# Performance work log

Measured on AMD Instinct MI355X. Metric: run time of the kernel, lower is better.

## Reference

```python
import jax, jax.numpy as jnp
import numpy as np

N_NODES = 100000
N_EDGES = 1600000
D = 128
BN_EPS = 1e-5

def setup_inputs() -> dict:
    key = jax.random.key(0)
    ks = jax.random.split(key, 6)
    h = jax.random.normal(ks[0], (N_NODES, D), dtype=jnp.float32)
    src = jax.random.randint(ks[1], (N_EDGES,), 0, N_NODES, dtype=jnp.int32)
    dst = jax.random.randint(ks[2], (N_EDGES,), 0, N_NODES, dtype=jnp.int32)
    eps = jnp.zeros((1,), dtype=jnp.float32)
    # 2-layer GIN apply_func MLP, scaled for stable activations
    W1 = jax.random.normal(ks[3], (D, D), dtype=jnp.float32) / np.sqrt(D)
    b1 = jnp.zeros((D,), dtype=jnp.float32)
    W2 = jax.random.normal(ks[4], (D, D), dtype=jnp.float32) / np.sqrt(D)
    b2 = jnp.zeros((D,), dtype=jnp.float32)
    gamma = jnp.ones((D,), dtype=jnp.float32)
    beta = jnp.zeros((D,), dtype=jnp.float32)
    return {"h": h, "src": src, "dst": dst, "eps": eps,
            "W1": W1, "b1": b1, "W2": W2, "b2": b2,
            "gamma": gamma, "beta": beta}

def reference(h, src, dst, eps, W1, b1, W2, b2, gamma, beta):
    # --- neighbor sum aggregation: update_all(copy_u('h'), fn.sum) ---
    msgs = h[src]                                   # [E, D] irregular gather
    neigh = jax.ops.segment_sum(msgs, dst, num_segments=N_NODES)  # [N, D]
    # --- eps-scaled self term ---
    x = (1.0 + eps[0]) * h + neigh                  # [N, D]
    # --- apply_func: 2-layer MLP ---
    x = jax.nn.relu(x @ W1 + b1)
    x = x @ W2 + b2
    # --- BatchNorm1d over node dim (training-mode batch stats) ---
    mean = jnp.mean(x, axis=0)
    var = jnp.mean(jnp.square(x - mean), axis=0)
    x = (x - mean) * jax.lax.rsqrt(var + BN_EPS) * gamma + beta
    # --- activation + residual ---
    x = jax.nn.relu(x)
    x = h + x  # residual (in_dim == out_dim)
    return x
```

## Files before the change

kernel.cpp:

```cpp
#include <hip/hip_runtime.h>

#define NN 100000
#define NE 1600000
#define DD 128
#define BN_EPS 1e-5f

#define NWIN 782
#define EPB 8192
#define NBLK ((NE + EPB - 1) / EPB)
#define CAP 3072

typedef __attribute__((ext_vector_type(8))) short short8;
typedef __attribute__((ext_vector_type(4))) float floatx4;

__device__ __forceinline__ unsigned short f2bf(float f) {
    union { float f; unsigned u; } v; v.f = f;
    return (unsigned short)((v.u + 0x7FFFu + ((v.u >> 16) & 1u)) >> 16);
}
__device__ __forceinline__ float bf2f(unsigned short u) {
    union { unsigned u; float f; } v; v.u = ((unsigned)u) << 16;
    return v.f;
}

__global__ __launch_bounds__(256) void prep_kernel(
    float* __restrict__ stats, int* __restrict__ wcnt,
    const float* __restrict__ W1, const float* __restrict__ W2,
    unsigned short* __restrict__ W1t, unsigned short* __restrict__ W2t,
    const float* __restrict__ h, unsigned short* __restrict__ hb, int do_hb)
{
    int tid0 = blockIdx.x * blockDim.x + threadIdx.x;
    int stride = gridDim.x * blockDim.x;
    if (tid0 < 2 * DD) stats[tid0] = 0.0f;
    if (tid0 < NWIN) wcnt[tid0] = 0;
    for (int i = tid0; i < DD * DD; i += stride) {
        int n = i >> 7, k = i & 127;
        W1t[i] = f2bf(W1[k * DD + n]);
        W2t[i] = f2bf(W2[k * DD + n]);
    }
    if (do_hb) {
        const float4* h4 = (const float4*)h;
        ushort4* hb4 = (ushort4*)hb;
        for (int i = tid0; i < NN * (DD / 4); i += stride) {
            float4 v = h4[i];
            ushort4 o;
            o.x = f2bf(v.x); o.y = f2bf(v.y); o.z = f2bf(v.z); o.w = f2bf(v.w);
            hb4[i] = o;
        }
    }
}

__global__ __launch_bounds__(256) void wscatter_kernel(
    const int* __restrict__ src, const int* __restrict__ dst,
    int* __restrict__ wcnt, int* __restrict__ estage)
{
    __shared__ int bins[NWIN];
    int blk = blockIdx.x, t = threadIdx.x;
    for (int j = t; j < NWIN; j += 256) bins[j] = 0;
    __syncthreads();
    int base = blk * EPB;
    int cnt = min(EPB, NE - base);
    for (int i = t; i < cnt; i += 256)
        atomicAdd(&bins[dst[base + i] >> 7], 1);
    __syncthreads();
    for (int j = t; j < NWIN; j += 256) {
        int c = bins[j];
        int b = (c > 0) ? atomicAdd(&wcnt[j], c) : 0;
        bins[j] = j * CAP + b;
    }
    __syncthreads();
    for (int i = t; i < cnt; i += 256) {
        int e = base + i;
        int d = dst[e];
        int pos = atomicAdd(&bins[d >> 7], 1);
        estage[pos] = (src[e] << 7) | (d & 127);
    }
}

__global__ __launch_bounds__(256) void wpermute_kernel(
    const int* __restrict__ wcnt, int* __restrict__ estage,
    int2* __restrict__ off2)
{
    __shared__ int ew[CAP];
    __shared__ int cnt[128];
    __shared__ int part[128];
    __shared__ int cur[128];
    int b = blockIdx.x, t = threadIdx.x;
    int wbase = b * CAP;
    int n = min(wcnt[b], CAP);
    if (t < 128) cnt[t] = 0;
    __syncthreads();
    for (int i = t; i < n; i += 256) {
        int e = estage[wbase + i];
        ew[i] = e;
        atomicAdd(&cnt[e & 127], 1);
    }
    __syncthreads();
    if (t < 128) part[t] = cnt[t];
    __syncthreads();
#pragma unroll
    for (int ofs = 1; ofs < 128; ofs <<= 1) {
        int u = (t < 128 && t >= ofs) ? part[t - ofs] : 0;
        __syncthreads();
        if (t < 128) part[t] += u;
        __syncthreads();
    }
    if (t < 128) {
        int excl = part[t] - cnt[t];
        cur[t] = wbase + excl;
        int node = (b << 7) + t;
        if (node < NN) off2[node] = make_int2(wbase + excl, wbase + excl + cnt[t]);
    }
    __syncthreads();
    for (int i = t; i < n; i += 256) {
        int e = ew[i];
        int pos = atomicAdd(&cur[e & 127], 1);
        estage[pos] = e >> 7;
    }
}

__global__ __launch_bounds__(256) void gather_bf16_kernel(
    const float* __restrict__ h, const unsigned short* __restrict__ hb,
    const float* __restrict__ eps, const int2* __restrict__ off2,
    const int* __restrict__ src_sorted, unsigned short* __restrict__ xb)
{
    int node = blockIdx.x * 16 + (threadIdx.x >> 4);
    if (node >= NN) return;
    int c8 = threadIdx.x & 15;
    const float s = 1.0f + eps[0];
    const float4* h4 = (const float4*)h;
    float4 a0 = h4[node * 32 + c8 * 2];
    float4 a1 = h4[node * 32 + c8 * 2 + 1];
    float acc[8] = {s * a0.x, s * a0.y, s * a0.z, s * a0.w,
                    s * a1.x, s * a1.y, s * a1.z, s * a1.w};
    int2 oo = off2[node];
    int e = oo.x, eend = oo.y;
    const short8* hb8 = (const short8*)hb;
    for (; e + 3 < eend; e += 4) {
        int s0 = src_sorted[e],     s1 = src_sorted[e + 1];
        int s2 = src_sorted[e + 2], s3 = src_sorted[e + 3];
        short8 v0 = hb8[s0 * 16 + c8];
        short8 v1 = hb8[s1 * 16 + c8];
        short8 v2 = hb8[s2 * 16 + c8];
        short8 v3 = hb8[s3 * 16 + c8];
#pragma unroll
        for (int j = 0; j < 8; ++j) {
            float t0 = bf2f((unsigned short)v0[j]) + bf2f((unsigned short)v1[j]);
            float t1 = bf2f((unsigned short)v2[j]) + bf2f((unsigned short)v3[j]);
            acc[j] += t0 + t1;
        }
    }
    for (; e < eend; ++e) {
        short8 v0 = hb8[src_sorted[e] * 16 + c8];
#pragma unroll
        for (int j = 0; j < 8; ++j) acc[j] += bf2f((unsigned short)v0[j]);
    }
    short8 o;
#pragma unroll
    for (int j = 0; j < 8; ++j) o[j] = (short)f2bf(acc[j]);
    ((short8*)xb)[node * 16 + c8] = o;
}

__global__ __launch_bounds__(256) void gather_f32_kernel(
    const float* __restrict__ h, const float* __restrict__ eps,
    const int2* __restrict__ off2, const int* __restrict__ src_sorted,
    unsigned short* __restrict__ xb)
{
    int node = blockIdx.x * 16 + (threadIdx.x >> 4);
    if (node >= NN) return;
    int c8 = threadIdx.x & 15;
    const float4* h4 = (const float4*)h;
    const float s = 1.0f + eps[0];
    float4 a0 = h4[node * 32 + c8 * 2];
    float4 a1 = h4[node * 32 + c8 * 2 + 1];
    float acc[8] = {s * a0.x, s * a0.y, s * a0.z, s * a0.w,
                    s * a1.x, s * a1.y, s * a1.z, s * a1.w};
    int2 oo = off2[node];
    int e = oo.x, eend = oo.y;
    for (; e + 1 < eend; e += 2) {
        int s0 = src_sorted[e], s1 = src_sorted[e + 1];
        float4 u0 = h4[s0 * 32 + c8 * 2], u1 = h4[s0 * 32 + c8 * 2 + 1];
        float4 w0 = h4[s1 * 32 + c8 * 2], w1 = h4[s1 * 32 + c8 * 2 + 1];
        acc[0] += u0.x + w0.x; acc[1] += u0.y + w0.y;
        acc[2] += u0.z + w0.z; acc[3] += u0.w + w0.w;
        acc[4] += u1.x + w1.x; acc[5] += u1.y + w1.y;
        acc[6] += u1.z + w1.z; acc[7] += u1.w + w1.w;
    }
    if (e < eend) {
        int s0 = src_sorted[e];
        float4 u0 = h4[s0 * 32 + c8 * 2], u1 = h4[s0 * 32 + c8 * 2 + 1];
        acc[0] += u0.x; acc[1] += u0.y; acc[2] += u0.z; acc[3] += u0.w;
        acc[4] += u1.x; acc[5] += u1.y; acc[6] += u1.z; acc[7] += u1.w;
    }
    short8 o;
#pragma unroll
    for (int j = 0; j < 8; ++j) o[j] = (short)f2bf(acc[j]);
    ((short8*)xb)[node * 16 + c8] = o;
}

__global__ __launch_bounds__(256) void mlp_fused_kernel(
    const unsigned short* __restrict__ X,
    const unsigned short* __restrict__ W1t, const unsigned short* __restrict__ W2t,
    const float* __restrict__ b1, const float* __restrict__ b2,
    unsigned short* __restrict__ Y, float* __restrict__ stats)
{
    extern __shared__ char smem[];
    unsigned short* wl = (unsigned short*)smem;
    unsigned short* xl = (unsigned short*)(smem + 34816);

    const int tid = threadIdx.x;
    const int r0 = blockIdx.x * 64;
    const int lane = tid & 63;
    const int wv = tid >> 6;
    const int m = lane & 15;
    const int hi = lane >> 4;

    const short8* W18 = (const short8*)W1t;
#pragma unroll
    for (int l = 0; l < 8; ++l) {
        int idx = tid + l * 256;
        int n = idx >> 4, c = idx & 15;
        *(short8*)&wl[n * 136 + c * 8] = W18[idx];
    }
    const short8* X8 = (const short8*)X;
#pragma unroll
    for (int l = 0; l < 4; ++l) {
        int idx = tid + l * 256;
        int row = idx >> 4, c = idx & 15;
        int g = r0 + row;
        short8 v = {0, 0, 0, 0, 0, 0, 0, 0};
        if (g < NN) v = X8[g * 16 + c];
        *(short8*)&xl[row * 136 + c * 8] = v;
    }
    __syncthreads();

    floatx4 acc[8];
#pragma unroll
    for (int i = 0; i < 8; ++i) acc[i] = (floatx4){0.f, 0.f, 0.f, 0.f};
#pragma unroll
    for (int kc = 0; kc < 4; ++kc) {
        short8 a = *(const short8*)&xl[(wv * 16 + m) * 136 + kc * 32 + hi * 8];
#pragma unroll
        for (int nt = 0; nt < 8; ++nt) {
            short8 b = *(const short8*)&wl[(nt * 16 + m) * 136 + kc * 32 + hi * 8];
            acc[nt] = __builtin_amdgcn_mfma_f32_16x16x32_bf16(a, b, acc[nt], 0, 0, 0);
        }
    }
    __syncthreads();

#pragma unroll
    for (int nt = 0; nt < 8; ++nt) {
        float bv = b1[nt * 16 + m];
#pragma unroll
        for (int r = 0; r < 4; ++r) {
            float v = fmaxf(acc[nt][r] + bv, 0.f);
            xl[(wv * 16 + hi * 4 + r) * 136 + nt * 16 + m] = f2bf(v);
        }
    }
    const short8* W28 = (const short8*)W2t;
#pragma unroll
    for (int l = 0; l < 8; ++l) {
        int idx = tid + l * 256;
        int n = idx >> 4, c = idx & 15;
        *(short8*)&wl[n * 136 + c * 8] = W28[idx];
    }
    __syncthreads();

#pragma unroll
    for (int i = 0; i < 8; ++i) acc[i] = (floatx4){0.f, 0.f, 0.f, 0.f};
#pragma unroll
    for (int kc = 0; kc < 4; ++kc) {
        short8 a = *(const short8*)&xl[(wv * 16 + m) * 136 + kc * 32 + hi * 8];
#pragma unroll
        for (int nt = 0; nt < 8; ++nt) {
            short8 b = *(const short8*)&wl[(nt * 16 + m) * 136 + kc * 32 + hi * 8];
            acc[nt] = __builtin_amdgcn_mfma_f32_16x16x32_bf16(a, b, acc[nt], 0, 0, 0);
        }
    }
    __syncthreads();

#pragma unroll
    for (int nt = 0; nt < 8; ++nt) {
        float bv = b2[nt * 16 + m];
#pragma unroll
        for (int r = 0; r < 4; ++r) {
            float v = acc[nt][r] + bv;
            xl[(wv * 16 + hi * 4 + r) * 136 + nt * 16 + m] = f2bf(v);
        }
    }
    __syncthreads();

#pragma unroll
    for (int l = 0; l < 4; ++l) {
        int idx = tid + l * 256;
        int row = idx >> 4, c = idx & 15;
        int g = r0 + row;
        if (g < NN)
            ((short8*)Y)[g * 16 + c] = *(const short8*)&xl[row * 136 + c * 8];
    }

    int col = tid & 127, half = tid >> 7;
    int rlim = min(64, NN - r0);
    int rbeg = half * 32, rend = min(rbeg + 32, rlim);
    float s = 0.f, q = 0.f;
    for (int r = rbeg; r < rend; ++r) {
        float v = bf2f(xl[r * 136 + col]);
        s += v; q += v * v;
    }
    float* red = (float*)wl;
    red[tid] = s;
    red[256 + tid] = q;
    __syncthreads();
    if (half == 0) {
        atomicAdd(&stats[col],      red[col] + red[128 + col]);
        atomicAdd(&stats[DD + col], red[256 + col] + red[256 + 128 + col]);
    }
}

__global__ __launch_bounds__(256) void bn_final_kernel(
    const unsigned short* __restrict__ Y, const float* __restrict__ h,
    const float* __restrict__ gamma, const float* __restrict__ beta,
    const float* __restrict__ stats, float* __restrict__ out)
{
    const float invN = 1.0f / (float)NN;
    const ushort4* Y4 = (const ushort4*)Y;
    const float4* H4 = (const float4*)h;
    float4* O4 = (float4*)out;
    const int total = NN * (DD / 4);
    for (int i = blockIdx.x * blockDim.x + threadIdx.x; i < total;
         i += gridDim.x * blockDim.x) {
        int cg = i & 31;
        int c = cg << 2;
        ushort4 u = Y4[i];
        float4 hv = H4[i];
        float4 g = ((const float4*)gamma)[cg];
        float4 bt = ((const float4*)beta)[cg];

        float m0 = stats[c + 0] * invN, m1 = stats[c + 1] * invN;
        float m2 = stats[c + 2] * invN, m3 = stats[c + 3] * invN;
        float v0 = stats[DD + c + 0] * invN - m0 * m0;
        float v1 = stats[DD + c + 1] * invN - m1 * m1;
        float v2 = stats[DD + c + 2] * invN - m2 * m2;
        float v3 = stats[DD + c + 3] * invN - m3 * m3;

        float4 r;
        r.x = hv.x + fmaxf((bf2f(u.x) - m0) * rsqrtf(v0 + BN_EPS) * g.x + bt.x, 0.f);
        r.y = hv.y + fmaxf((bf2f(u.y) - m1) * rsqrtf(v1 + BN_EPS) * g.y + bt.y, 0.f);
        r.z = hv.z + fmaxf((bf2f(u.z) - m2) * rsqrtf(v2 + BN_EPS) * g.z + bt.z, 0.f);
        r.w = hv.w + fmaxf((bf2f(u.w) - m3) * rsqrtf(v3 + BN_EPS) * g.w + bt.w, 0.f);
        O4[i] = r;
    }
}

extern "C" void kernel_launch(void* const* d_in, const int* in_sizes, int n_in,
                              void* d_out, int out_size, void* d_ws, size_t ws_size,
                              hipStream_t stream)
{
    const float* h     = (const float*)d_in[0];
    const int*   src   = (const int*)d_in[1];
    const int*   dst   = (const int*)d_in[2];
    const float* eps   = (const float*)d_in[3];
    const float* W1    = (const float*)d_in[4];
    const float* b1    = (const float*)d_in[5];
    const float* W2    = (const float*)d_in[6];
    const float* b2    = (const float*)d_in[7];
    const float* gamma = (const float*)d_in[8];
    const float* beta  = (const float*)d_in[9];
    float* out = (float*)d_out;

    char* w = (char*)d_ws;
    size_t o = 0;
    int2* off2      = (int2*)(w + o); o += (size_t)NN * 8;
    float* stats    = (float*)(w + o); o += 256 * 4;
    unsigned short* W1t = (unsigned short*)(w + o); o += (size_t)DD * DD * 2;
    unsigned short* W2t = (unsigned short*)(w + o); o += (size_t)DD * DD * 2;
    int* wcnt       = (int*)(w + o); o += 1024 * 4;
    int* estage     = (int*)(w + o); o += (size_t)NWIN * CAP * 4;
    unsigned short* xb  = (unsigned short*)(w + o); o += (size_t)NN * DD * 2;
    unsigned short* hb  = (unsigned short*)(w + o); o += (size_t)NN * DD * 2;
    const int use_hb = (ws_size >= o) ? 1 : 0;

    prep_kernel<<<512, 256, 0, stream>>>(stats, wcnt, W1, W2, W1t, W2t, h, hb, use_hb);

    wscatter_kernel<<<NBLK, 256, 0, stream>>>(src, dst, wcnt, estage);

    wpermute_kernel<<<NWIN, 256, 0, stream>>>(wcnt, estage, off2);

    if (use_hb)
        gather_bf16_kernel<<<(NN + 15) / 16, 256, 0, stream>>>(h, hb, eps, off2, estage, xb);
    else
        gather_f32_kernel<<<(NN + 15) / 16, 256, 0, stream>>>(h, eps, off2, estage, xb);

    int gemm_blocks = (NN + 63) / 64;
    size_t gemm_lds = 34816 + 17408;
    mlp_fused_kernel<<<gemm_blocks, 256, gemm_lds, stream>>>(xb, W1t, W2t, b1, b2, xb, stats);

    bn_final_kernel<<<1024, 256, 0, stream>>>(xb, h, gamma, beta, stats, out);
}
```

Measured before the change: 322.1 us.

## Fuse prep with edge scatter, fuse window permute with gather, streamline BN epilogue

The weight/h conversion now runs as extra blocks inside the edge-binning launch, and dst indices are cached in LDS for the second pass. The per-window permutation is merged into the gather kernel, which keeps sorted sources in LDS instead of writing them and an offset array back to global memory. The BN kernel precomputes per-column scale and shift and uses 8-wide loads. This saves launches and global round trips, but the gather runs with far fewer, larger blocks (128 nodes each), which may hurt load balance and latency hiding.

```diff
diff --git a/kernel.cpp b/kernel.cpp
--- a/kernel.cpp
+++ b/kernel.cpp
@@ -9,6 +9,9 @@
 #define EPB 8192
 #define NBLK ((NE + EPB - 1) / EPB)
 #define CAP 3072
+#define PREPBLKS 316
+#define GRID_PS (NBLK + PREPBLKS)
+#define BN_BLOCKS 1024
 
 typedef __attribute__((ext_vector_type(8))) short short8;
 typedef __attribute__((ext_vector_type(4))) float floatx4;
@@ -22,179 +25,169 @@
     return v.f;
 }
 
-__global__ __launch_bounds__(256) void prep_kernel(
-    float* __restrict__ stats, int* __restrict__ wcnt,
+__global__ __launch_bounds__(256) void prep_scatter_kernel(
+    float* __restrict__ stats,
     const float* __restrict__ W1, const float* __restrict__ W2,
     unsigned short* __restrict__ W1t, unsigned short* __restrict__ W2t,
-    const float* __restrict__ h, unsigned short* __restrict__ hb, int do_hb)
-{
-    int tid0 = blockIdx.x * blockDim.x + threadIdx.x;
-    int stride = gridDim.x * blockDim.x;
-    if (tid0 < 2 * DD) stats[tid0] = 0.0f;
-    if (tid0 < NWIN) wcnt[tid0] = 0;
-    for (int i = tid0; i < DD * DD; i += stride) {
-        int n = i >> 7, k = i & 127;
-        W1t[i] = f2bf(W1[k * DD + n]);
-        W2t[i] = f2bf(W2[k * DD + n]);
-    }
-    if (do_hb) {
-        const float4* h4 = (const float4*)h;
-        ushort4* hb4 = (ushort4*)hb;
-        for (int i = tid0; i < NN * (DD / 4); i += stride) {
-            float4 v = h4[i];
-            ushort4 o;
-            o.x = f2bf(v.x); o.y = f2bf(v.y); o.z = f2bf(v.z); o.w = f2bf(v.w);
-            hb4[i] = o;
-        }
-    }
-}
-
-__global__ __launch_bounds__(256) void wscatter_kernel(
+    const float* __restrict__ h, unsigned short* __restrict__ hb, int do_hb,
     const int* __restrict__ src, const int* __restrict__ dst,
     int* __restrict__ wcnt, int* __restrict__ estage)
 {
     __shared__ int bins[NWIN];
-    int blk = blockIdx.x, t = threadIdx.x;
-    for (int j = t; j < NWIN; j += 256) bins[j] = 0;
-    __syncthreads();
-    int base = blk * EPB;
-    int cnt = min(EPB, NE - base);
-    for (int i = t; i < cnt; i += 256)
-        atomicAdd(&bins[dst[base + i] >> 7], 1);
-    __syncthreads();
-    for (int j = t; j < NWIN; j += 256) {
-        int c = bins[j];
-        int b = (c > 0) ? atomicAdd(&wcnt[j], c) : 0;
-        bins[j] = j * CAP + b;
-    }
-    __syncthreads();
-    for (int i = t; i < cnt; i += 256) {
-        int e = base + i;
-        int d = dst[e];
-        int pos = atomicAdd(&bins[d >> 7], 1);
-        estage[pos] = (src[e] << 7) | (d & 127);
-    }
-}
-
-__global__ __launch_bounds__(256) void wpermute_kernel(
-    const int* __restrict__ wcnt, int* __restrict__ estage,
-    int2* __restrict__ off2)
+    __shared__ int dstl[EPB];
+    int t = threadIdx.x;
+
+    if (blockIdx.x < NBLK) {
+        int blk = blockIdx.x;
+        for (int j = t; j < NWIN; j += 256) bins[j] = 0;
+        __syncthreads();
+        int base = blk * EPB;
+        int cnt = min(EPB, NE - base);
+        for (int i = t; i < cnt; i += 256) {
+            int d = dst[base + i];
+            dstl[i] = d;
+            atomicAdd(&bins[d >> 7], 1);
+        }
+        __syncthreads();
+        for (int j = t; j < NWIN; j += 256) {
+            int c = bins[j];
+            int b = (c > 0) ? atomicAdd(&wcnt[j], c) : 0;
+            bins[j] = j * CAP + b;
+        }
+        __syncthreads();
+        for (int i = t; i < cnt; i += 256) {
+            int d = dstl[i];
+            int pos = atomicAdd(&bins[d >> 7], 1);
+            estage[pos] = (src[base + i] << 7) | (d & 127);
+        }
+    } else {
+        int tid0 = (blockIdx.x - NBLK) * 256 + t;
+        int stride = PREPBLKS * 256;
+        if (tid0 < 2 * DD) stats[tid0] = 0.0f;
+        for (int i = tid0; i < DD * DD; i += stride) {
+            int n = i >> 7, k = i & 127;
+            W1t[i] = f2bf(W1[k * DD + n]);
+            W2t[i] = f2bf(W2[k * DD + n]);
+        }
+        if (do_hb) {
+            const float4* h4 = (const float4*)h;
+            ushort4* hb4 = (ushort4*)hb;
+            for (int i = tid0; i < NN * (DD / 4); i += stride) {
+                float4 v = h4[i];
+                ushort4 o;
+                o.x = f2bf(v.x); o.y = f2bf(v.y); o.z = f2bf(v.z); o.w = f2bf(v.w);
+                hb4[i] = o;
+            }
+        }
+    }
+}
+
+template <bool HB>
+__global__ __launch_bounds__(512) void permgather_kernel(
+    const float* __restrict__ h, const unsigned short* __restrict__ hb,
+    const float* __restrict__ eps, const int* __restrict__ wcnt,
+    const int* __restrict__ estage, unsigned short* __restrict__ xb)
 {
     __shared__ int ew[CAP];
+    __shared__ int es[CAP];
     __shared__ int cnt[128];
-    __shared__ int part[128];
+    __shared__ int scn[128];
+    __shared__ int begS[128];
+    __shared__ int endS[128];
     __shared__ int cur[128];
+
     int b = blockIdx.x, t = threadIdx.x;
+    if (t < 128) cnt[t] = 0;
+    __syncthreads();
+
+    int n = min(wcnt[b], CAP);
     int wbase = b * CAP;
-    int n = min(wcnt[b], CAP);
-    if (t < 128) cnt[t] = 0;
-    __syncthreads();
-    for (int i = t; i < n; i += 256) {
+    for (int i = t; i < n; i += 512) {
         int e = estage[wbase + i];
         ew[i] = e;
         atomicAdd(&cnt[e & 127], 1);
     }
     __syncthreads();
-    if (t < 128) part[t] = cnt[t];
+
+    if (t < 128) scn[t] = cnt[t];
     __syncthreads();
 #pragma unroll
     for (int ofs = 1; ofs < 128; ofs <<= 1) {
-        int u = (t < 128 && t >= ofs) ? part[t - ofs] : 0;
-        __syncthreads();
-        if (t < 128) part[t] += u;
+        int u = (t < 128 && t >= ofs) ? scn[t - ofs] : 0;
+        __syncthreads();
+        if (t < 128) scn[t] += u;
         __syncthreads();
     }
     if (t < 128) {
-        int excl = part[t] - cnt[t];
-        cur[t] = wbase + excl;
-        int node = (b << 7) + t;
-        if (node < NN) off2[node] = make_int2(wbase + excl, wbase + excl + cnt[t]);
-    }
-    __syncthreads();
-    for (int i = t; i < n; i += 256) {
+        int excl = scn[t] - cnt[t];
+        begS[t] = excl;
+        endS[t] = excl + cnt[t];
+        cur[t] = excl;
+    }
+    __syncthreads();
+
+    for (int i = t; i < n; i += 512) {
         int e = ew[i];
         int pos = atomicAdd(&cur[e & 127], 1);
-        estage[pos] = e >> 7;
-    }
-}
-
-__global__ __launch_bounds__(256) void gather_bf16_kernel(
-    const float* __restrict__ h, const unsigned short* __restrict__ hb,
-    const float* __restrict__ eps, const int2* __restrict__ off2,
-    const int* __restrict__ src_sorted, unsigned short* __restrict__ xb)
-{
-    int node = blockIdx.x * 16 + (threadIdx.x >> 4);
-    if (node >= NN) return;
-    int c8 = threadIdx.x & 15;
-    const float s = 1.0f + eps[0];
+        es[pos] = e >> 7;
+    }
+    __syncthreads();
+
+    const float sE = 1.0f + eps[0];
     const float4* h4 = (const float4*)h;
-    float4 a0 = h4[node * 32 + c8 * 2];
-    float4 a1 = h4[node * 32 + c8 * 2 + 1];
-    float acc[8] = {s * a0.x, s * a0.y, s * a0.z, s * a0.w,
-                    s * a1.x, s * a1.y, s * a1.z, s * a1.w};
-    int2 oo = off2[node];
-    int e = oo.x, eend = oo.y;
     const short8* hb8 = (const short8*)hb;
-    for (; e + 3 < eend; e += 4) {
-        int s0 = src_sorted[e],     s1 = src_sorted[e + 1];
-        int s2 = src_sorted[e + 2], s3 = src_sorted[e + 3];
-        short8 v0 = hb8[s0 * 16 + c8];
-        short8 v1 = hb8[s1 * 16 + c8];
-        short8 v2 = hb8[s2 * 16 + c8];
-        short8 v3 = hb8[s3 * 16 + c8];
-#pragma unroll
-        for (int j = 0; j < 8; ++j) {
-            float t0 = bf2f((unsigned short)v0[j]) + bf2f((unsigned short)v1[j]);
-            float t1 = bf2f((unsigned short)v2[j]) + bf2f((unsigned short)v3[j]);
-            acc[j] += t0 + t1;
-        }
-    }
-    for (; e < eend; ++e) {
-        short8 v0 = hb8[src_sorted[e] * 16 + c8];
-#pragma unroll
-        for (int j = 0; j < 8; ++j) acc[j] += bf2f((unsigned short)v0[j]);
-    }
-    short8 o;
-#pragma unroll
-    for (int j = 0; j < 8; ++j) o[j] = (short)f2bf(acc[j]);
-    ((short8*)xb)[node * 16 + c8] = o;
-}
-
-__global__ __launch_bounds__(256) void gather_f32_kernel(
-    const float* __restrict__ h, const float* __restrict__ eps,
-    const int2* __restrict__ off2, const int* __restrict__ src_sorted,
-    unsigned short* __restrict__ xb)
-{
-    int node = blockIdx.x * 16 + (threadIdx.x >> 4);
-    if (node >= NN) return;
-    int c8 = threadIdx.x & 15;
-    const float4* h4 = (const float4*)h;
-    const float s = 1.0f + eps[0];
-    float4 a0 = h4[node * 32 + c8 * 2];
-    float4 a1 = h4[node * 32 + c8 * 2 + 1];
-    float acc[8] = {s * a0.x, s * a0.y, s * a0.z, s * a0.w,
-                    s * a1.x, s * a1.y, s * a1.z, s * a1.w};
-    int2 oo = off2[node];
-    int e = oo.x, eend = oo.y;
-    for (; e + 1 < eend; e += 2) {
-        int s0 = src_sorted[e], s1 = src_sorted[e + 1];
-        float4 u0 = h4[s0 * 32 + c8 * 2], u1 = h4[s0 * 32 + c8 * 2 + 1];
-        float4 w0 = h4[s1 * 32 + c8 * 2], w1 = h4[s1 * 32 + c8 * 2 + 1];
-        acc[0] += u0.x + w0.x; acc[1] += u0.y + w0.y;
-        acc[2] += u0.z + w0.z; acc[3] += u0.w + w0.w;
-        acc[4] += u1.x + w1.x; acc[5] += u1.y + w1.y;
-        acc[6] += u1.z + w1.z; acc[7] += u1.w + w1.w;
-    }
-    if (e < eend) {
-        int s0 = src_sorted[e];
-        float4 u0 = h4[s0 * 32 + c8 * 2], u1 = h4[s0 * 32 + c8 * 2 + 1];
-        acc[0] += u0.x; acc[1] += u0.y; acc[2] += u0.z; acc[3] += u0.w;
-        acc[4] += u1.x; acc[5] += u1.y; acc[6] += u1.z; acc[7] += u1.w;
-    }
-    short8 o;
-#pragma unroll
-    for (int j = 0; j < 8; ++j) o[j] = (short)f2bf(acc[j]);
-    ((short8*)xb)[node * 16 + c8] = o;
+    int c8 = t & 15;
+#pragma unroll
+    for (int pass = 0; pass < 4; ++pass) {
+        int nl = pass * 32 + (t >> 4);
+        int node = (b << 7) + nl;
+        if (node >= NN) continue;
+        float4 a0 = h4[node * 32 + c8 * 2];
+        float4 a1 = h4[node * 32 + c8 * 2 + 1];
+        float acc[8] = {sE * a0.x, sE * a0.y, sE * a0.z, sE * a0.w,
+                        sE * a1.x, sE * a1.y, sE * a1.z, sE * a1.w};
+        int e = begS[nl], eend = endS[nl];
+        if (HB) {
+            for (; e + 3 < eend; e += 4) {
+                int s0 = es[e], s1 = es[e + 1], s2 = es[e + 2], s3 = es[e + 3];
+                short8 v0 = hb8[s0 * 16 + c8];
+                short8 v1 = hb8[s1 * 16 + c8];
+                short8 v2 = hb8[s2 * 16 + c8];
+                short8 v3 = hb8[s3 * 16 + c8];
+#pragma unroll
+                for (int j = 0; j < 8; ++j) {
+                    float t0 = bf2f((unsigned short)v0[j]) + bf2f((unsigned short)v1[j]);
+                    float t1 = bf2f((unsigned short)v2[j]) + bf2f((unsigned short)v3[j]);
+                    acc[j] += t0 + t1;
+                }
+            }
+            for (; e < eend; ++e) {
+                short8 v0 = hb8[es[e] * 16 + c8];
+#pragma unroll
+                for (int j = 0; j < 8; ++j) acc[j] += bf2f((unsigned short)v0[j]);
+            }
+        } else {
+            for (; e + 1 < eend; e += 2) {
+                int s0 = es[e], s1 = es[e + 1];
+                float4 u0 = h4[s0 * 32 + c8 * 2], u1 = h4[s0 * 32 + c8 * 2 + 1];
+                float4 w0 = h4[s1 * 32 + c8 * 2], w1 = h4[s1 * 32 + c8 * 2 + 1];
+                acc[0] += u0.x + w0.x; acc[1] += u0.y + w0.y;
+                acc[2] += u0.z + w0.z; acc[3] += u0.w + w0.w;
+                acc[4] += u1.x + w1.x; acc[5] += u1.y + w1.y;
+                acc[6] += u1.z + w1.z; acc[7] += u1.w + w1.w;
+            }
+            if (e < eend) {
+                int s0 = es[e];
+                float4 u0 = h4[s0 * 32 + c8 * 2], u1 = h4[s0 * 32 + c8 * 2 + 1];
+                acc[0] += u0.x; acc[1] += u0.y; acc[2] += u0.z; acc[3] += u0.w;
+                acc[4] += u1.x; acc[5] += u1.y; acc[6] += u1.z; acc[7] += u1.w;
+            }
+        }
+        short8 o;
+#pragma unroll
+        for (int j = 0; j < 8; ++j) o[j] = (short)f2bf(acc[j]);
+        ((short8*)xb)[node * 16 + c8] = o;
+    }
 }
 
 __global__ __launch_bounds__(256) void mlp_fused_kernel(
@@ -322,32 +315,37 @@
     const float* __restrict__ stats, float* __restrict__ out)
 {
     const float invN = 1.0f / (float)NN;
-    const ushort4* Y4 = (const ushort4*)Y;
+    int t0 = blockIdx.x * 256 + threadIdx.x;
+    int c8 = t0 & 15;
+    float sc[8], sh[8];
+#pragma unroll
+    for (int j = 0; j < 8; ++j) {
+        int col = c8 * 8 + j;
+        float mu = stats[col] * invN;
+        float var = stats[DD + col] * invN - mu * mu;
+        float s = rsqrtf(var + BN_EPS) * gamma[col];
+        sc[j] = s;
+        sh[j] = beta[col] - mu * s;
+    }
+    const short8* Y8 = (const short8*)Y;
     const float4* H4 = (const float4*)h;
     float4* O4 = (float4*)out;
-    const int total = NN * (DD / 4);
-    for (int i = blockIdx.x * blockDim.x + threadIdx.x; i < total;
-         i += gridDim.x * blockDim.x) {
-        int cg = i & 31;
-        int c = cg << 2;
-        ushort4 u = Y4[i];
-        float4 hv = H4[i];
-        float4 g = ((const float4*)gamma)[cg];
-        float4 bt = ((const float4*)beta)[cg];
-
-        float m0 = stats[c + 0] * invN, m1 = stats[c + 1] * invN;
-        float m2 = stats[c + 2] * invN, m3 = stats[c + 3] * invN;
-        float v0 = stats[DD + c + 0] * invN - m0 * m0;
-        float v1 = stats[DD + c + 1] * invN - m1 * m1;
-        float v2 = stats[DD + c + 2] * invN - m2 * m2;
-        float v3 = stats[DD + c + 3] * invN - m3 * m3;
-
-        float4 r;
-        r.x = hv.x + fmaxf((bf2f(u.x) - m0) * rsqrtf(v0 + BN_EPS) * g.x + bt.x, 0.f);
-        r.y = hv.y + fmaxf((bf2f(u.y) - m1) * rsqrtf(v1 + BN_EPS) * g.y + bt.y, 0.f);
-        r.z = hv.z + fmaxf((bf2f(u.z) - m2) * rsqrtf(v2 + BN_EPS) * g.z + bt.z, 0.f);
-        r.w = hv.w + fmaxf((bf2f(u.w) - m3) * rsqrtf(v3 + BN_EPS) * g.w + bt.w, 0.f);
-        O4[i] = r;
+    const int total = NN * 16;
+    const int stride = BN_BLOCKS * 256;
+    for (int i = t0; i < total; i += stride) {
+        short8 u = Y8[i];
+        float4 h0 = H4[2 * i], h1 = H4[2 * i + 1];
+        float4 r0, r1;
+        r0.x = h0.x + fmaxf(bf2f((unsigned short)u[0]) * sc[0] + sh[0], 0.f);
+        r0.y = h0.y + fmaxf(bf2f((unsigned short)u[1]) * sc[1] + sh[1], 0.f);
+        r0.z = h0.z + fmaxf(bf2f((unsigned short)u[2]) * sc[2] + sh[2], 0.f);
+        r0.w = h0.w + fmaxf(bf2f((unsigned short)u[3]) * sc[3] + sh[3], 0.f);
+        r1.x = h1.x + fmaxf(bf2f((unsigned short)u[4]) * sc[4] + sh[4], 0.f);
+        r1.y = h1.y + fmaxf(bf2f((unsigned short)u[5]) * sc[5] + sh[5], 0.f);
+        r1.z = h1.z + fmaxf(bf2f((unsigned short)u[6]) * sc[6] + sh[6], 0.f);
+        r1.w = h1.w + fmaxf(bf2f((unsigned short)u[7]) * sc[7] + sh[7], 0.f);
+        O4[2 * i] = r0;
+        O4[2 * i + 1] = r1;
     }
 }
 
@@ -369,30 +367,28 @@
 
     char* w = (char*)d_ws;
     size_t o = 0;
-    int2* off2      = (int2*)(w + o); o += (size_t)NN * 8;
     float* stats    = (float*)(w + o); o += 256 * 4;
+    int* wcnt       = (int*)(w + o); o += 1024 * 4;
     unsigned short* W1t = (unsigned short*)(w + o); o += (size_t)DD * DD * 2;
     unsigned short* W2t = (unsigned short*)(w + o); o += (size_t)DD * DD * 2;
-    int* wcnt       = (int*)(w + o); o += 1024 * 4;
     int* estage     = (int*)(w + o); o += (size_t)NWIN * CAP * 4;
     unsigned short* xb  = (unsigned short*)(w + o); o += (size_t)NN * DD * 2;
     unsigned short* hb  = (unsigned short*)(w + o); o += (size_t)NN * DD * 2;
     const int use_hb = (ws_size >= o) ? 1 : 0;
 
-    prep_kernel<<<512, 256, 0, stream>>>(stats, wcnt, W1, W2, W1t, W2t, h, hb, use_hb);
-
-    wscatter_kernel<<<NBLK, 256, 0, stream>>>(src, dst, wcnt, estage);
-
-    wpermute_kernel<<<NWIN, 256, 0, stream>>>(wcnt, estage, off2);
+    hipMemsetAsync(wcnt, 0, 1024 * sizeof(int), stream);
+
+    prep_scatter_kernel<<<GRID_PS, 256, 0, stream>>>(
+        stats, W1, W2, W1t, W2t, h, hb, use_hb, src, dst, wcnt, estage);
 
     if (use_hb)
-        gather_bf16_kernel<<<(NN + 15) / 16, 256, 0, stream>>>(h, hb, eps, off2, estage, xb);
+        permgather_kernel<true><<<NWIN, 512, 0, stream>>>(h, hb, eps, wcnt, estage, xb);
     else
-        gather_f32_kernel<<<(NN + 15) / 16, 256, 0, stream>>>(h, eps, off2, estage, xb);
+        permgather_kernel<false><<<NWIN, 512, 0, stream>>>(h, hb, eps, wcnt, estage, xb);
 
     int gemm_blocks = (NN + 63) / 64;
     size_t gemm_lds = 34816 + 17408;
     mlp_fused_kernel<<<gemm_blocks, 256, gemm_lds, stream>>>(xb, W1t, W2t, b1, b2, xb, stats);
 
-    bn_final_kernel<<<1024, 256, 0, stream>>>(xb, h, gamma, beta, stats, out);
-}
+    bn_final_kernel<<<BN_BLOCKS, 256, 0, stream>>>(xb, h, gamma, beta, stats, out);
+}
```

Result: faster. 298.2 us (-7.4%).
